# Kernel optimization log

Hardware: AMD Instinct MI355X
Metric: run time of the kernel (lower is better)

Reference implementation:

```python
import jax, jax.numpy as jnp
import numpy as np

B = 4; S_L = 512; WIN = 256; SCH = 3; CCH = 128; F = 8; P = 4; RNN = 128; FC = 256
L1 = (WIN - F + 1) // P          # after conv1 + pool1
L2 = (L1 - F + 1) // P           # after conv2 + pool2
D1 = L2 * CCH                    # flattened conv feature dim fed to GRU


def _conv1d(x, w, b):
    # x: (N, W, Cin), w: (F, Cin, Cout), VALID, stride 1 (matches keras Conv1D)
    return jax.lax.conv_general_dilated(x, w, (1,), 'VALID', dimension_numbers=('NWC', 'WIO', 'NWC')) + b


def _maxpool(x, p):
    return jax.lax.reduce_window(x, -jnp.inf, jax.lax.max, (1, p, 1), (1, p, 1), 'VALID')


def _gru(x, h0, mask, W, U, b):
    # keras GRU v2 (reset_after=True). b[0]=input bias, b[1]=recurrent bias.
    # Masked steps carry state through (keras semantics: output==state for GRU).
    u = U.shape[0]
    xg = x @ W + b[0]  # (B, T, 3u) precomputed input projections
    br = b[1]

    def step(h, inp):
        xt, mt = inp  # (B, 3u), (B,)
        rg = h @ U + br
        z = jax.nn.sigmoid(xt[:, :u] + rg[:, :u])
        r = jax.nn.sigmoid(xt[:, u:2 * u] + rg[:, u:2 * u])
        hh = jnp.tanh(xt[:, 2 * u:] + r * rg[:, 2 * u:])
        hn = z * h + (1.0 - z) * hh
        hn = jnp.where(mt[:, None], hn, h)
        return hn, hn

    _, ys = jax.lax.scan(step, h0, (jnp.swapaxes(xg, 0, 1), jnp.swapaxes(mask, 0, 1)))
    return jnp.swapaxes(ys, 0, 1)  # (B, T, u)


def _bidir(x, m, hf, hb, Wf, Uf, bf, Wb, Ub, bb):
    # Bidirectional(merge='concat'); backward layer sees reversed inputs+mask,
    # its output is reversed back to align with time (keras behaviour).
    yf = _gru(x, hf, m, Wf, Uf, bf)
    yb = _gru(x[:, ::-1], hb, m[:, ::-1], Wb, Ub, bb)[:, ::-1]
    return jnp.concatenate([yf, yb], axis=-1)


def _forward(x, state1_f, state1_b, state2_f, state2_b,
             conv1_w, conv1_b, conv2_w, conv2_b,
             g1f_W, g1f_U, g1f_b, g1b_W, g1b_U, g1b_b,
             g2f_W, g2f_U, g2f_b, g2b_W, g2b_U, g2b_b,
             d1_w, d1_b, d2_w, d2_b, d3_w, d3_b, m):
    bsz = x.shape[0]
    h = x.reshape(bsz * S_L, WIN, SCH)
    h = _maxpool(jax.nn.leaky_relu(_conv1d(h, conv1_w, conv1_b), 0.2), P)
    h = _maxpool(jax.nn.leaky_relu(_conv1d(h, conv2_w, conv2_b), 0.2), P)
    h = h.reshape(bsz, S_L, D1)
    h = _bidir(h, m, state1_f, state1_b, g1f_W, g1f_U, g1f_b, g1b_W, g1b_U, g1b_b)
    h = _bidir(h, m, state2_f, state2_b, g2f_W, g2f_U, g2f_b, g2b_W, g2b_U, g2b_b)
    # keras layers.Attention(use_scale=False): dot-product self attention,
    # key mask -> -1e9 on scores, query mask -> zero outputs.
    scores = jnp.einsum('btd,bsd->bts', h, h)
    scores = jnp.where(m[:, None, :], scores, -1e9)
    h = jnp.einsum('bts,bsd->btd', jax.nn.softmax(scores, axis=-1), h)
    h = h * m[:, :, None].astype(h.dtype)
    h = jax.nn.leaky_relu(h @ d1_w + d1_b, 0.2)   # dropout is identity at inference
    h = jax.nn.leaky_relu(h @ d2_w + d2_b, 0.2)
    return (h @ d3_w + d3_b)[..., 0]              # squeeze -> (B, s_l)


def setup_inputs() -> dict:
    key = jax.random.key(0)
    ks = jax.random.split(key, 32)
    g = lambda k, s: jax.random.normal(k, s, jnp.float32) * 0.05
    inp = {}
    inp['x'] = jax.random.normal(ks[0], (B, S_L, WIN, SCH), jnp.float32)
    inp['m'] = jax.random.randint(ks[1], (B, S_L), 0, 2) > 0
    inp['state1_f'] = jax.random.uniform(ks[2], (B, RNN), jnp.float32, -1.0, 1.0)
    inp['state1_b'] = jax.random.uniform(ks[3], (B, RNN), jnp.float32, -1.0, 1.0)
    inp['state2_f'] = jax.random.uniform(ks[4], (B, RNN), jnp.float32, -1.0, 1.0)
    inp['state2_b'] = jax.random.uniform(ks[5], (B, RNN), jnp.float32, -1.0, 1.0)
    inp['conv1_w'] = g(ks[6], (F, SCH, CCH)); inp['conv1_b'] = jnp.zeros((CCH,), jnp.float32)
    inp['conv2_w'] = g(ks[7], (F, CCH, CCH)); inp['conv2_b'] = jnp.zeros((CCH,), jnp.float32)
    i = 8
    for nm, din in (('g1f', D1), ('g1b', D1), ('g2f', 2 * RNN), ('g2b', 2 * RNN)):
        inp[nm + '_W'] = g(ks[i], (din, 3 * RNN))
        inp[nm + '_U'] = g(ks[i + 1], (RNN, 3 * RNN))
        inp[nm + '_b'] = jnp.zeros((2, 3 * RNN), jnp.float32)
        i += 2
    inp['d1_w'] = g(ks[i], (2 * RNN, FC)); inp['d1_b'] = jnp.zeros((FC,), jnp.float32)
    inp['d2_w'] = g(ks[i + 1], (FC, FC)); inp['d2_b'] = jnp.zeros((FC,), jnp.float32)
    inp['d3_w'] = g(ks[i + 2], (FC, 1)); inp['d3_b'] = jnp.zeros((1,), jnp.float32)
    return inp


def reference(x, m, state1_f, state1_b, state2_f, state2_b,
              conv1_w, conv1_b, conv2_w, conv2_b,
              g1f_W, g1f_U, g1f_b, g1b_W, g1b_U, g1b_b,
              g2f_W, g2f_U, g2f_b, g2b_W, g2b_U, g2b_b,
              d1_w, d1_b, d2_w, d2_b, d3_w, d3_b):
    return _forward(x, state1_f, state1_b, state2_f, state2_b,
                    conv1_w, conv1_b, conv2_w, conv2_b,
                    g1f_W, g1f_U, g1f_b, g1b_W, g1b_U, g1b_b,
                    g2f_W, g2f_U, g2f_b, g2b_W, g2b_U, g2b_b,
                    d1_w, d1_b, d2_w, d2_b, d3_w, d3_b, m)
```

## Files before the change

kernel.cpp:

```cpp
#include <hip/hip_runtime.h>

#define LRELU(v) ((v) > 0.f ? (v) : 0.2f * (v))

typedef float f32x4 __attribute__((ext_vector_type(4)));
typedef __bf16 bf16x8 __attribute__((ext_vector_type(8)));
typedef unsigned short ushort8v __attribute__((ext_vector_type(8)));
typedef unsigned int u32x2 __attribute__((ext_vector_type(2)));

__device__ __forceinline__ unsigned short f2bf(float f) {
    unsigned int u = __float_as_uint(f);
    u += 0x7fffu + ((u >> 16) & 1u);
    return (unsigned short)(u >> 16);
}
__device__ __forceinline__ float bf2f(unsigned short h) {
    return __uint_as_float(((unsigned int)h) << 16);
}
__device__ __forceinline__ float sigmoid_fast(float x) {
    float e = __builtin_amdgcn_exp2f(-x * 1.442695041f);
    return __builtin_amdgcn_rcpf(1.f + e);
}
__device__ __forceinline__ float tanh_fast(float x) {
    float e = __builtin_amdgcn_exp2f(x * 2.885390082f);
    return 1.f - 2.f * __builtin_amdgcn_rcpf(e + 1.f);
}
__device__ __forceinline__ float dpp_add_xor1(float v) {
    int r = __builtin_amdgcn_mov_dpp(__float_as_int(v), 0xB1, 0xF, 0xF, true);
    return v + __int_as_float(r);
}
__device__ __forceinline__ float dpp_add_xor2(float v) {
    int r = __builtin_amdgcn_mov_dpp(__float_as_int(v), 0x4E, 0xF, 0xF, true);
    return v + __int_as_float(r);
}

__device__ __forceinline__ void wtpack(const float* __restrict__ W,
                                       unsigned short* __restrict__ h,
                                       unsigned short* __restrict__ l, int K,
                                       int N, long idx) {
    int n = (int)(idx / K), k = (int)(idx % K);
    float v = W[(long)k * N + n];
    unsigned short hi = f2bf(v);
    h[idx] = hi;
    l[idx] = f2bf(v - bf2f(hi));
}
__device__ __forceinline__ void ugpack(const float* __restrict__ U,
                                       float* __restrict__ up, int widx) {
    int quad = widx >> 11;
    int rem = widx & 2047;
    int t = rem >> 2, i = rem & 3;
    int g = quad >> 3, q = quad & 7;
    int c = t >> 2, kq = t & 3;
    up[widx] = U[(long)(kq * 32 + q * 4 + i) * 384 + g * 128 + c];
}

__global__ __launch_bounds__(256) void prepack_all(
    const float* __restrict__ w2, unsigned short* __restrict__ bth,
    unsigned short* __restrict__ btl, const float* __restrict__ g1fW,
    unsigned short* __restrict__ wt1fh, unsigned short* __restrict__ wt1fl,
    const float* __restrict__ g1bW, unsigned short* __restrict__ wt1bh,
    unsigned short* __restrict__ wt1bl, const float* __restrict__ g2fW,
    unsigned short* __restrict__ wt2fh, unsigned short* __restrict__ wt2fl,
    const float* __restrict__ g2bW, unsigned short* __restrict__ wt2bh,
    unsigned short* __restrict__ wt2bl, const float* __restrict__ g1fU,
    float* __restrict__ up1f, const float* __restrict__ g1bU,
    float* __restrict__ up1b, const float* __restrict__ g2fU,
    float* __restrict__ up2f, const float* __restrict__ g2bU,
    float* __restrict__ up2b, const float* __restrict__ d1w,
    unsigned short* __restrict__ d1th, unsigned short* __restrict__ d1tl,
    const float* __restrict__ d2w, unsigned short* __restrict__ d2th,
    unsigned short* __restrict__ d2tl, const unsigned int* __restrict__ mraw,
    int* __restrict__ mi) {
    const int bid = blockIdx.x, tid = threadIdx.x;
    if (bid < 512) {
        int idx = bid * 256 + tid;
        int c = idx >> 10, k = idx & 1023;
        float v = w2[k * 128 + c];
        unsigned short hi = f2bf(v);
        bth[(long)c * 1024 + k] = hi;
        btl[(long)c * 1024 + k] = f2bf(v - bf2f(hi));
    } else if (bid < 3008) {
        wtpack(g1fW, wt1fh, wt1fl, 1664, 384, (long)(bid - 512) * 256 + tid);
    } else if (bid < 5504) {
        wtpack(g1bW, wt1bh, wt1bl, 1664, 384, (long)(bid - 3008) * 256 + tid);
    } else if (bid < 5888) {
        wtpack(g2fW, wt2fh, wt2fl, 256, 384, (long)(bid - 5504) * 256 + tid);
    } else if (bid < 6272) {
        wtpack(g2bW, wt2bh, wt2bl, 256, 384, (long)(bid - 5888) * 256 + tid);
    } else if (bid < 6464) {
        ugpack(g1fU, up1f, (bid - 6272) * 256 + tid);
    } else if (bid < 6656) {
        ugpack(g1bU, up1b, (bid - 6464) * 256 + tid);
    } else if (bid < 6848) {
        ugpack(g2fU, up2f, (bid - 6656) * 256 + tid);
    } else if (bid < 7040) {
        ugpack(g2bU, up2b, (bid - 6848) * 256 + tid);
    } else if (bid < 7296) {
        wtpack(d1w, d1th, d1tl, 256, 256, (long)(bid - 7040) * 256 + tid);
    } else if (bid < 7552) {
        wtpack(d2w, d2th, d2tl, 256, 256, (long)(bid - 7296) * 256 + tid);
    } else {
        __shared__ int flag;
        if (tid == 0) flag = 0;
        __syncthreads();
        unsigned a = mraw[tid * 2], bb = mraw[tid * 2 + 1];
        if (a > 1u || bb > 1u) flag = 1;
        __syncthreads();
        if (flag) {
            const unsigned char* b8 = (const unsigned char*)mraw;
            for (int i = tid; i < 2048; i += 256) mi[i] = b8[i] ? 1 : 0;
        } else {
            for (int i = tid; i < 2048; i += 256) mi[i] = mraw[i] ? 1 : 0;
        }
    }
}

__global__ __launch_bounds__(256) void conv_kernel(
    const float* __restrict__ x, const float* __restrict__ w1,
    const float* __restrict__ b1, const unsigned short* __restrict__ bth,
    const unsigned short* __restrict__ btl, const float* __restrict__ b2,
    unsigned short* __restrict__ feat_h, unsigned short* __restrict__ feat_l) {
    __shared__ float xs[3][256];
    __shared__ __align__(16) unsigned short p1h[72 * 128];
    __shared__ __align__(16) unsigned short p1l[72 * 128];
    long s = blockIdx.x;
    int tid = threadIdx.x;
    const float* xp = x + s * 768;
    for (int i = tid; i < 768; i += 256) xs[i % 3][i / 3] = xp[i];
    for (int i = tid; i < 10 * 128; i += 256) {
        p1h[62 * 128 + i] = 0;
        p1l[62 * 128 + i] = 0;
    }
    __syncthreads();

    {
        int ch = tid & 127;
        int half = tid >> 7;
        float w1r[24];
#pragma unroll
        for (int fc = 0; fc < 24; fc++) w1r[fc] = w1[fc * 128 + ch];
        float bias1 = b1[ch];
        for (int po = half; po < 62; po += 2) {
            int p0 = po * 4;
            float a0 = bias1, a1 = bias1, a2 = bias1, a3 = bias1;
#pragma unroll
            for (int c = 0; c < 3; c++) {
                float xv[11];
#pragma unroll
                for (int q = 0; q < 11; q++) xv[q] = xs[c][p0 + q];
#pragma unroll
                for (int f = 0; f < 8; f++) {
                    float w = w1r[f * 3 + c];
                    a0 = fmaf(xv[f + 0], w, a0);
                    a1 = fmaf(xv[f + 1], w, a1);
                    a2 = fmaf(xv[f + 2], w, a2);
                    a3 = fmaf(xv[f + 3], w, a3);
                }
            }
            float m01 = fmaxf(LRELU(a0), LRELU(a1));
            float m23 = fmaxf(LRELU(a2), LRELU(a3));
            float v = fmaxf(m01, m23);
            unsigned short hi = f2bf(v);
            unsigned short lo = f2bf(v - bf2f(hi));
            int cs = ch ^ ((po & 7) << 3);
            p1h[po * 128 + cs] = hi;
            p1l[po * 128 + cs] = lo;
        }
    }
    __syncthreads();

    const int l = tid & 63, w = tid >> 6;
    const int r = l & 15, g = l >> 4;
    f32x4 acc[4][2];
    const f32x4 zz = {0.f, 0.f, 0.f, 0.f};
#pragma unroll
    for (int m = 0; m < 4; m++) {
        acc[m][0] = zz;
        acc[m][1] = zz;
    }
#pragma unroll 2
    for (int ks = 0; ks < 32; ks++) {
        const int f = ks >> 2;
        const int cin0 = ((ks & 3) << 5) + (g << 3);
        bf16x8 bh[2], bl[2];
#pragma unroll
        for (int n = 0; n < 2; n++) {
            const int c = ((w << 1) + n) * 16 + r;
            const long bo = (long)c * 1024 + (ks << 5) + (g << 3);
            bh[n] = __builtin_bit_cast(bf16x8, *(const ushort8v*)(bth + bo));
            bl[n] = __builtin_bit_cast(bf16x8, *(const ushort8v*)(btl + bo));
        }
        bf16x8 ah[4], al[4];
#pragma unroll
        for (int m = 0; m < 4; m++) {
            const int row = m * 16 + r + f;
            const int col = cin0 ^ ((row & 7) << 3);
            const int off = row * 128 + col;
            ah[m] = __builtin_bit_cast(bf16x8, *(const ushort8v*)(p1h + off));
            al[m] = __builtin_bit_cast(bf16x8, *(const ushort8v*)(p1l + off));
        }
#pragma unroll
        for (int m = 0; m < 4; m++) {
#pragma unroll
            for (int n = 0; n < 2; n++) {
                acc[m][n] = __builtin_amdgcn_mfma_f32_16x16x32_bf16(ah[m], bh[n], acc[m][n], 0, 0, 0);
                acc[m][n] = __builtin_amdgcn_mfma_f32_16x16x32_bf16(ah[m], bl[n], acc[m][n], 0, 0, 0);
                acc[m][n] = __builtin_amdgcn_mfma_f32_16x16x32_bf16(al[m], bh[n], acc[m][n], 0, 0, 0);
            }
        }
    }
#pragma unroll
    for (int m = 0; m < 4; m++) {
        const int j = m * 4 + g;
        if (j < 13) {
#pragma unroll
            for (int n = 0; n < 2; n++) {
                const int ch = ((w << 1) + n) * 16 + r;
                const float bias = b2[ch];
                float v0 = LRELU(acc[m][n].x + bias);
                float v1 = LRELU(acc[m][n].y + bias);
                float v2 = LRELU(acc[m][n].z + bias);
                float v3 = LRELU(acc[m][n].w + bias);
                float v = fmaxf(fmaxf(v0, v1), fmaxf(v2, v3));
                unsigned short hi = f2bf(v);
                feat_h[s * 1664 + j * 128 + ch] = hi;
                feat_l[s * 1664 + j * 128 + ch] = f2bf(v - bf2f(hi));
            }
        }
    }
}

__global__ __launch_bounds__(256) void gemm_proj(
    const unsigned short* __restrict__ Agh, const unsigned short* __restrict__ Agl,
    const unsigned short* __restrict__ B0h, const unsigned short* __restrict__ B0l,
    const unsigned short* __restrict__ B1h, const unsigned short* __restrict__ B1l,
    const float* __restrict__ bias0, const float* __restrict__ bias1,
    float* __restrict__ C0, float* __restrict__ C1, int M, int N, int K) {
    const int z = blockIdx.z;
    const unsigned short* __restrict__ Bth = z ? B1h : B0h;
    const unsigned short* __restrict__ Btl = z ? B1l : B0l;
    const float* __restrict__ bias = z ? bias1 : bias0;
    float* __restrict__ C = z ? C1 : C0;
    __shared__ __align__(16) unsigned short Ahs[2][64 * 32];
    __shared__ __align__(16) unsigned short Als[2][64 * 32];
    const int tid = threadIdx.x;
    const int w = tid >> 6, l = tid & 63, r = l & 15, g = l >> 4;
    const int m0 = blockIdx.y * 64, n0 = blockIdx.x * 64;
    const int col = n0 + w * 16 + r;
    const int srow = tid >> 2, sgq = tid & 3;
    f32x4 acc[4];
    const f32x4 zzv = {0.f, 0.f, 0.f, 0.f};
#pragma unroll
    for (int m = 0; m < 4; m++) acc[m] = zzv;

    const long abase = (long)(m0 + srow) * K + ((sgq ^ (srow & 3)) << 3);
    auto stage = [&](int k0, int buf) {
        __builtin_amdgcn_global_load_lds(
            (const __attribute__((address_space(1))) void*)(Agh + abase + k0),
            (__attribute__((address_space(3))) void*)&Ahs[buf][tid * 8], 16, 0, 0);
        __builtin_amdgcn_global_load_lds(
            (const __attribute__((address_space(1))) void*)(Agl + abase + k0),
            (__attribute__((address_space(3))) void*)&Als[buf][tid * 8], 16, 0, 0);
    };
    stage(0, 0);
    const long bbase = (long)col * K + g * 8;
    ushort8v bhc = *(const ushort8v*)(Bth + bbase);
    ushort8v blc = *(const ushort8v*)(Btl + bbase);

    for (int k0 = 0; k0 < K; k0 += 32) {
        const int buf = (k0 >> 5) & 1;
        asm volatile("s_waitcnt vmcnt(0)" ::: "memory");
        __builtin_amdgcn_s_barrier();
        ushort8v nbh, nbl;
        if (k0 + 32 < K) {
            stage(k0 + 32, buf ^ 1);
            nbh = *(const ushort8v*)(Bth + bbase + k0 + 32);
            nbl = *(const ushort8v*)(Btl + bbase + k0 + 32);
        }
        bf16x8 bh = __builtin_bit_cast(bf16x8, bhc);
        bf16x8 bl = __builtin_bit_cast(bf16x8, blc);
#pragma unroll
        for (int m = 0; m < 4; m++) {
            const int arow = m * 16 + r;
            const int aoff = arow * 32 + ((g ^ (arow & 3)) << 3);
            bf16x8 ah = __builtin_bit_cast(bf16x8, *(const ushort8v*)(&Ahs[buf][aoff]));
            bf16x8 al = __builtin_bit_cast(bf16x8, *(const ushort8v*)(&Als[buf][aoff]));
            acc[m] = __builtin_amdgcn_mfma_f32_16x16x32_bf16(ah, bh, acc[m], 0, 0, 0);
            acc[m] = __builtin_amdgcn_mfma_f32_16x16x32_bf16(ah, bl, acc[m], 0, 0, 0);
            acc[m] = __builtin_amdgcn_mfma_f32_16x16x32_bf16(al, bh, acc[m], 0, 0, 0);
        }
        bhc = nbh;
        blc = nbl;
    }
    const float bv = bias[col];
#pragma unroll
    for (int m = 0; m < 4; m++) {
#pragma unroll
        for (int q = 0; q < 4; q++) {
            const int row = m0 + m * 16 + g * 4 + q;
            C[(long)row * N + col] = acc[m][q] + bv;
        }
    }
}

__global__ __launch_bounds__(256) void gemm_scores(
    const unsigned short* __restrict__ Hh, const unsigned short* __restrict__ Hl,
    const int* __restrict__ mask, float* __restrict__ S) {
    const int bz = blockIdx.z;
    const unsigned short* __restrict__ Agh = Hh + (long)bz * 512 * 256;
    const unsigned short* __restrict__ Agl = Hl + (long)bz * 512 * 256;
    float* __restrict__ C = S + (long)bz * 512 * 512;
    const int K = 256, N = 512;
    __shared__ __align__(16) unsigned short Ahs[2][64 * 32];
    __shared__ __align__(16) unsigned short Als[2][64 * 32];
    const int tid = threadIdx.x;
    const int w = tid >> 6, l = tid & 63, r = l & 15, g = l >> 4;
    const int m0 = blockIdx.y * 64, n0 = blockIdx.x * 64;
    const int col = n0 + w * 16 + r;
    const int srow = tid >> 2, sgq = tid & 3;
    f32x4 acc[4];
    const f32x4 zzv = {0.f, 0.f, 0.f, 0.f};
#pragma unroll
    for (int m = 0; m < 4; m++) acc[m] = zzv;

    const long abase = (long)(m0 + srow) * K + ((sgq ^ (srow & 3)) << 3);
    auto stage = [&](int k0, int buf) {
        __builtin_amdgcn_global_load_lds(
            (const __attribute__((address_space(1))) void*)(Agh + abase + k0),
            (__attribute__((address_space(3))) void*)&Ahs[buf][tid * 8], 16, 0, 0);
        __builtin_amdgcn_global_load_lds(
            (const __attribute__((address_space(1))) void*)(Agl + abase + k0),
            (__attribute__((address_space(3))) void*)&Als[buf][tid * 8], 16, 0, 0);
    };
    stage(0, 0);
    const long bbase = (long)col * K + g * 8;
    ushort8v bhc = *(const ushort8v*)(Agh + bbase);
    ushort8v blc = *(const ushort8v*)(Agl + bbase);

    for (int k0 = 0; k0 < K; k0 += 32) {
        const int buf = (k0 >> 5) & 1;
        asm volatile("s_waitcnt vmcnt(0)" ::: "memory");
        __builtin_amdgcn_s_barrier();
        ushort8v nbh, nbl;
        if (k0 + 32 < K) {
            stage(k0 + 32, buf ^ 1);
            nbh = *(const ushort8v*)(Agh + bbase + k0 + 32);
            nbl = *(const ushort8v*)(Agl + bbase + k0 + 32);
        }
        bf16x8 bh = __builtin_bit_cast(bf16x8, bhc);
        bf16x8 bl = __builtin_bit_cast(bf16x8, blc);
#pragma unroll
        for (int m = 0; m < 4; m++) {
            const int arow = m * 16 + r;
            const int aoff = arow * 32 + ((g ^ (arow & 3)) << 3);
            bf16x8 ah = __builtin_bit_cast(bf16x8, *(const ushort8v*)(&Ahs[buf][aoff]));
            bf16x8 al = __builtin_bit_cast(bf16x8, *(const ushort8v*)(&Als[buf][aoff]));
            acc[m] = __builtin_amdgcn_mfma_f32_16x16x32_bf16(ah, bh, acc[m], 0, 0, 0);
            acc[m] = __builtin_amdgcn_mfma_f32_16x16x32_bf16(ah, bl, acc[m], 0, 0, 0);
            acc[m] = __builtin_amdgcn_mfma_f32_16x16x32_bf16(al, bh, acc[m], 0, 0, 0);
        }
        bhc = nbh;
        blc = nbl;
    }
    const int mk = mask[bz * 512 + col];
#pragma unroll
    for (int m = 0; m < 4; m++) {
#pragma unroll
        for (int q = 0; q < 4; q++) {
            const int row = m0 + m * 16 + g * 4 + q;
            float v = acc[m][q];
            C[(long)row * N + col] = mk ? v : -1e9f;
        }
    }
}

template <int ACT, int QMASK>
__global__ __launch_bounds__(256) void gemm_v3(
    const unsigned short* __restrict__ Agh, const unsigned short* __restrict__ Agl,
    const unsigned short* __restrict__ Bth, const unsigned short* __restrict__ Btl,
    const float* __restrict__ bias, const int* __restrict__ qmask,
    unsigned short* __restrict__ Ch, unsigned short* __restrict__ Cl,
    long sA, long sB, long sC, int M, int N, int K) {
    const int bz = blockIdx.z;
    Agh += (long)bz * sA;
    Agl += (long)bz * sA;
    Bth += (long)bz * sB;
    Btl += (long)bz * sB;
    Ch += (long)bz * sC;
    Cl += (long)bz * sC;
    __shared__ __align__(16) unsigned short Ahs[2][64 * 32];
    __shared__ __align__(16) unsigned short Als[2][64 * 32];
    const int tid = threadIdx.x;
    const int w = tid >> 6, l = tid & 63, r = l & 15, g = l >> 4;
    const int m0 = blockIdx.y * 64, n0 = blockIdx.x * 64;
    const int col = n0 + w * 16 + r;
    const int srow = tid >> 2, sgq = tid & 3;
    f32x4 acc[4];
    const f32x4 zzv = {0.f, 0.f, 0.f, 0.f};
#pragma unroll
    for (int m = 0; m < 4; m++) acc[m] = zzv;

    const long abase = (long)(m0 + srow) * K + ((sgq ^ (srow & 3)) << 3);
    auto stage = [&](int k0, int buf) {
        __builtin_amdgcn_global_load_lds(
            (const __attribute__((address_space(1))) void*)(Agh + abase + k0),
            (__attribute__((address_space(3))) void*)&Ahs[buf][tid * 8], 16, 0, 0);
        __builtin_amdgcn_global_load_lds(
            (const __attribute__((address_space(1))) void*)(Agl + abase + k0),
            (__attribute__((address_space(3))) void*)&Als[buf][tid * 8], 16, 0, 0);
    };
    stage(0, 0);
    const long bbase = (long)col * K + g * 8;
    ushort8v bhc = *(const ushort8v*)(Bth + bbase);
    ushort8v blc = *(const ushort8v*)(Btl + bbase);

    for (int k0 = 0; k0 < K; k0 += 32) {
        const int buf = (k0 >> 5) & 1;
        asm volatile("s_waitcnt vmcnt(0)" ::: "memory");
        __builtin_amdgcn_s_barrier();
        ushort8v nbh, nbl;
        if (k0 + 32 < K) {
            stage(k0 + 32, buf ^ 1);
            nbh = *(const ushort8v*)(Bth + bbase + k0 + 32);
            nbl = *(const ushort8v*)(Btl + bbase + k0 + 32);
        }
        bf16x8 bh = __builtin_bit_cast(bf16x8, bhc);
        bf16x8 bl = __builtin_bit_cast(bf16x8, blc);
#pragma unroll
        for (int m = 0; m < 4; m++) {
            const int arow = m * 16 + r;
            const int aoff = arow * 32 + ((g ^ (arow & 3)) << 3);
            bf16x8 ah = __builtin_bit_cast(bf16x8, *(const ushort8v*)(&Ahs[buf][aoff]));
            bf16x8 al = __builtin_bit_cast(bf16x8, *(const ushort8v*)(&Als[buf][aoff]));
            acc[m] = __builtin_amdgcn_mfma_f32_16x16x32_bf16(ah, bh, acc[m], 0, 0, 0);
            acc[m] = __builtin_amdgcn_mfma_f32_16x16x32_bf16(ah, bl, acc[m], 0, 0, 0);
            acc[m] = __builtin_amdgcn_mfma_f32_16x16x32_bf16(al, bh, acc[m], 0, 0, 0);
        }
        bhc = nbh;
        blc = nbl;
    }
    const float bv = bias ? bias[col] : 0.f;
#pragma unroll
    for (int m = 0; m < 4; m++) {
#pragma unroll
        for (int q = 0; q < 4; q++) {
            const int row = m0 + m * 16 + g * 4 + q;
            float v = acc[m][q] + bv;
            if (ACT == 1) v = LRELU(v);
            if (QMASK) v *= (float)qmask[bz * M + row];
            unsigned short hi = f2bf(v);
            Ch[(long)row * N + col] = hi;
            Cl[(long)row * N + col] = f2bf(v - bf2f(hi));
        }
    }
}

__global__ __launch_bounds__(256) void transpose_hl(
    const unsigned short* __restrict__ inh, const unsigned short* __restrict__ inl,
    unsigned short* __restrict__ outh, unsigned short* __restrict__ outl) {
    __shared__ unsigned short th[32][33], tl[32][33];
    const int b = blockIdx.z;
    const int s0 = blockIdx.x * 32, d0 = blockIdx.y * 32;
    const unsigned short* ih = inh + (long)b * 512 * 256;
    const unsigned short* il = inl + (long)b * 512 * 256;
    unsigned short* oh = outh + (long)b * 256 * 512;
    unsigned short* ol = outl + (long)b * 256 * 512;
    const int tx = threadIdx.x & 31, ty = threadIdx.x >> 5;
#pragma unroll
    for (int i = 0; i < 4; i++) {
        int s = s0 + ty + i * 8;
        th[ty + i * 8][tx] = ih[(long)s * 256 + d0 + tx];
        tl[ty + i * 8][tx] = il[(long)s * 256 + d0 + tx];
    }
    __syncthreads();
#pragma unroll
    for (int i = 0; i < 4; i++) {
        int d = d0 + ty + i * 8;
        oh[(long)d * 512 + s0 + tx] = th[tx][ty + i * 8];
        ol[(long)d * 512 + s0 + tx] = tl[tx][ty + i * 8];
    }
}

__global__ __launch_bounds__(256) void softmax_kernel(
    const float* __restrict__ S, unsigned short* __restrict__ Ph,
    unsigned short* __restrict__ Pl) {
    long row = blockIdx.x;
    const float* p = S + row * 512;
    int tid = threadIdx.x;
    __shared__ float red[8];
    float v0 = p[tid], v1 = p[tid + 256];
    float mx = fmaxf(v0, v1);
#pragma unroll
    for (int off = 32; off; off >>= 1) mx = fmaxf(mx, __shfl_down(mx, off));
    if ((tid & 63) == 0) red[tid >> 6] = mx;
    __syncthreads();
    mx = fmaxf(fmaxf(red[0], red[1]), fmaxf(red[2], red[3]));
    float e0 = expf(v0 - mx), e1 = expf(v1 - mx);
    float sm = e0 + e1;
#pragma unroll
    for (int off = 32; off; off >>= 1) sm += __shfl_down(sm, off);
    if ((tid & 63) == 0) red[4 + (tid >> 6)] = sm;
    __syncthreads();
    float inv = 1.f / (red[4] + red[5] + red[6] + red[7]);
    float w0 = e0 * inv, w1 = e1 * inv;
    unsigned short h0 = f2bf(w0), h1 = f2bf(w1);
    Ph[row * 512 + tid] = h0;
    Pl[row * 512 + tid] = f2bf(w0 - bf2f(h0));
    Ph[row * 512 + tid + 256] = h1;
    Pl[row * 512 + tid + 256] = f2bf(w1 - bf2f(h1));
}

#define D4(a0, a1, hv, uv)           \
    a0 = fmaf(hv.x, uv.x, a0);       \
    a1 = fmaf(hv.y, uv.y, a1);       \
    a0 = fmaf(hv.z, uv.z, a0);       \
    a1 = fmaf(hv.w, uv.w, a1);

__global__ __launch_bounds__(512, 2) void gru_kernel(
    const float* __restrict__ xgf, const float* __restrict__ xgb,
    const float* __restrict__ Upf, const float* __restrict__ Upb,
    const float* __restrict__ brf, const float* __restrict__ brb,
    const float* __restrict__ h0f, const float* __restrict__ h0b,
    const int* __restrict__ mask, unsigned short* __restrict__ outh,
    unsigned short* __restrict__ outl) {
    int b = blockIdx.x & 3;
    int dir = blockIdx.x >> 2;
    const float* __restrict__ xg = dir ? xgb : xgf;
    const float* __restrict__ Up = dir ? Upb : Upf;
    const float* __restrict__ br = dir ? brb : brf;
    const float* __restrict__ h0 = dir ? h0b : h0f;
    const int tid = threadIdx.x;
    const int c = tid >> 2;
    const int kq = tid & 3;

    __shared__ __align__(16) float xs[2][16 * 384];
    __shared__ __align__(16) float hsh[2][144];
    __shared__ __align__(16) unsigned int histp[16][128];
    __shared__ unsigned long long mwords[8];

    auto stage = [&](int cc, int bufi) {
#pragma unroll
        for (int i = 0; i < 3; i++) {
            int g = i * 512 + tid;
            int j = g / 96;
            int col = (g - j * 96) * 4;
            int ts = cc * 16 + j;
            int t = dir ? (511 - ts) : ts;
            const float* src = xg + ((long)(b * 512 + t)) * 384 + col;
            __builtin_amdgcn_global_load_lds(
                (const __attribute__((address_space(1))) void*)src,
                (__attribute__((address_space(3))) void*)&xs[bufi][g * 4], 16, 0, 0);
        }
    };
    stage(0, 0);

    const float* ub = Up + (tid << 2);
    f32x4 uz0 = *(const f32x4*)(ub + 0 * 2048);
    f32x4 uz1 = *(const f32x4*)(ub + 1 * 2048);
    f32x4 uz2 = *(const f32x4*)(ub + 2 * 2048);
    f32x4 uz3 = *(const f32x4*)(ub + 3 * 2048);
    f32x4 uz4 = *(const f32x4*)(ub + 4 * 2048);
    f32x4 uz5 = *(const f32x4*)(ub + 5 * 2048);
    f32x4 uz6 = *(const f32x4*)(ub + 6 * 2048);
    f32x4 uz7 = *(const f32x4*)(ub + 7 * 2048);
    f32x4 ur0 = *(const f32x4*)(ub + 8 * 2048);
    f32x4 ur1 = *(const f32x4*)(ub + 9 * 2048);
    f32x4 ur2 = *(const f32x4*)(ub + 10 * 2048);
    f32x4 ur3 = *(const f32x4*)(ub + 11 * 2048);
    f32x4 ur4 = *(const f32x4*)(ub + 12 * 2048);
    f32x4 ur5 = *(const f32x4*)(ub + 13 * 2048);
    f32x4 ur6 = *(const f32x4*)(ub + 14 * 2048);
    f32x4 ur7 = *(const f32x4*)(ub + 15 * 2048);
    f32x4 uh0 = *(const f32x4*)(ub + 16 * 2048);
    f32x4 uh1 = *(const f32x4*)(ub + 17 * 2048);
    f32x4 uh2 = *(const f32x4*)(ub + 18 * 2048);
    f32x4 uh3 = *(const f32x4*)(ub + 19 * 2048);
    f32x4 uh4 = *(const f32x4*)(ub + 20 * 2048);
    f32x4 uh5 = *(const f32x4*)(ub + 21 * 2048);
    f32x4 uh6 = *(const f32x4*)(ub + 22 * 2048);
    f32x4 uh7 = *(const f32x4*)(ub + 23 * 2048);

    float br3[3];
#pragma unroll
    for (int g = 0; g < 3; g++) br3[g] = br[g * 128 + c];

    float hreg = h0[b * 128 + c];
    if (kq == 0) hsh[0][c + (c >> 5) * 4] = hreg;
    if (tid < 64) {
#pragma unroll
        for (int w = 0; w < 8; w++) {
            int idx = w * 64 + tid;
            int t = dir ? (511 - idx) : idx;
            unsigned long long bm = __ballot(mask[b * 512 + t] != 0);
            if (tid == 0) mwords[w] = bm;
        }
    }
    asm volatile("s_waitcnt lgkmcnt(0)" ::: "memory");
    __builtin_amdgcn_s_barrier();

    int cur = 0;
    for (int cc = 0; cc < 32; cc++) {
        asm volatile("s_waitcnt vmcnt(0)" ::: "memory");
        if (cc < 31) stage(cc + 1, (cc + 1) & 1);
        __builtin_amdgcn_s_barrier();
        const float* xb = xs[cc & 1];
        unsigned mwbits = (unsigned)((mwords[cc >> 2] >> ((cc & 3) * 16)) & 0xffffull);
#pragma unroll 1
        for (int jj = 0; jj < 16; jj++) {
            if ((mwbits >> jj) & 1) {
                const float* hp = &hsh[cur][kq * 36];
                float4 h0v = *(const float4*)(hp + 0);
                float4 h1v = *(const float4*)(hp + 4);
                float4 h2v = *(const float4*)(hp + 8);
                float4 h3v = *(const float4*)(hp + 12);
                float4 h4v = *(const float4*)(hp + 16);
                float4 h5v = *(const float4*)(hp + 20);
                float4 h6v = *(const float4*)(hp + 24);
                float4 h7v = *(const float4*)(hp + 28);
                float az0 = 0.f, az1 = 0.f, ar0 = 0.f, ar1 = 0.f, ah0 = 0.f, ah1 = 0.f;
                D4(az0, az1, h0v, uz0) D4(az0, az1, h1v, uz1)
                D4(az0, az1, h2v, uz2) D4(az0, az1, h3v, uz3)
                D4(az0, az1, h4v, uz4) D4(az0, az1, h5v, uz5)
                D4(az0, az1, h6v, uz6) D4(az0, az1, h7v, uz7)
                D4(ar0, ar1, h0v, ur0) D4(ar0, ar1, h1v, ur1)
                D4(ar0, ar1, h2v, ur2) D4(ar0, ar1, h3v, ur3)
                D4(ar0, ar1, h4v, ur4) D4(ar0, ar1, h5v, ur5)
                D4(ar0, ar1, h6v, ur6) D4(ar0, ar1, h7v, ur7)
                D4(ah0, ah1, h0v, uh0) D4(ah0, ah1, h1v, uh1)
                D4(ah0, ah1, h2v, uh2) D4(ah0, ah1, h3v, uh3)
                D4(ah0, ah1, h4v, uh4) D4(ah0, ah1, h5v, uh5)
                D4(ah0, ah1, h6v, uh6) D4(ah0, ah1, h7v, uh7)
                float rgz = dpp_add_xor2(dpp_add_xor1(az0 + az1));
                float rgr = dpp_add_xor2(dpp_add_xor1(ar0 + ar1));
                float rgh = dpp_add_xor2(dpp_add_xor1(ah0 + ah1));
                if (kq == 0) {
                    float xz = xb[jj * 384 + c];
                    float xr = xb[jj * 384 + 128 + c];
                    float xh = xb[jj * 384 + 256 + c];
                    float z = sigmoid_fast(xz + rgz + br3[0]);
                    float r_ = sigmoid_fast(xr + rgr + br3[1]);
                    float hc = tanh_fast(fmaf(r_, rgh + br3[2], xh));
                    float hn = fmaf(z, hreg - hc, hc);
                    hreg = hn;
                    hsh[cur ^ 1][c + (c >> 5) * 4] = hn;
                    unsigned short hh = f2bf(hn);
                    histp[jj][c] = (unsigned)hh |
                                   ((unsigned)f2bf(hn - bf2f(hh)) << 16);
                }
                asm volatile("s_waitcnt lgkmcnt(0)" ::: "memory");
                __builtin_amdgcn_s_barrier();
                cur ^= 1;
            } else {
                if (kq == 0) {
                    unsigned short hh = f2bf(hreg);
                    histp[jj][c] = (unsigned)hh |
                                   ((unsigned)f2bf(hreg - bf2f(hh)) << 16);
                }
            }
        }
        asm volatile("s_waitcnt lgkmcnt(0)" ::: "memory");
        __builtin_amdgcn_s_barrier();
        {
            int fj = tid >> 5, fc = (tid & 31) << 2;
            int ts2 = cc * 16 + fj;
            int tf = dir ? (511 - ts2) : ts2;
            long ob = ((long)(b * 512 + tf)) * 256 + dir * 128 + fc;
            uint4 hp4 = *(const uint4*)&histp[fj][fc];
            u32x2 ph, pl;
            ph.x = (hp4.x & 0xffffu) | (hp4.y << 16);
            ph.y = (hp4.z & 0xffffu) | (hp4.w << 16);
            pl.x = (hp4.x >> 16) | (hp4.y & 0xffff0000u);
            pl.y = (hp4.z >> 16) | (hp4.w & 0xffff0000u);
            *(u32x2*)(outh + ob) = ph;
            *(u32x2*)(outl + ob) = pl;
        }
    }
}

__global__ __launch_bounds__(256) void final_kernel(
    const unsigned short* __restrict__ fh, const unsigned short* __restrict__ fl,
    const float* __restrict__ w, const float* __restrict__ b,
    float* __restrict__ out) {
    int row = blockIdx.x * 4 + (threadIdx.x >> 6);
    int lane = threadIdx.x & 63;
    const unsigned short* ah = fh + (long)row * 256;
    const unsigned short* al = fl + (long)row * 256;
    float acc = 0.f;
#pragma unroll
    for (int i = 0; i < 4; i++) {
        int idx = lane + i * 64;
        float a = bf2f(ah[idx]) + bf2f(al[idx]);
        acc = fmaf(a, w[idx], acc);
    }
#pragma unroll
    for (int off = 32; off; off >>= 1) acc += __shfl_down(acc, off);
    if (lane == 0) out[row] = acc + b[0];
}

extern "C" void kernel_launch(void* const* d_in, const int* in_sizes, int n_in,
                              void* d_out, int out_size, void* d_ws,
                              size_t ws_size, hipStream_t stream) {
    const float* x = (const float*)d_in[0];
    const unsigned int* mraw = (const unsigned int*)d_in[1];
    const float* s1f = (const float*)d_in[2];
    const float* s1b = (const float*)d_in[3];
    const float* s2f = (const float*)d_in[4];
    const float* s2b = (const float*)d_in[5];
    const float* c1w = (const float*)d_in[6];
    const float* c1b = (const float*)d_in[7];
    const float* c2w = (const float*)d_in[8];
    const float* c2b = (const float*)d_in[9];
    const float* g1fW = (const float*)d_in[10];
    const float* g1fU = (const float*)d_in[11];
    const float* g1fb = (const float*)d_in[12];
    const float* g1bW = (const float*)d_in[13];
    const float* g1bU = (const float*)d_in[14];
    const float* g1bb = (const float*)d_in[15];
    const float* g2fW = (const float*)d_in[16];
    const float* g2fU = (const float*)d_in[17];
    const float* g2fb = (const float*)d_in[18];
    const float* g2bW = (const float*)d_in[19];
    const float* g2bU = (const float*)d_in[20];
    const float* g2bb = (const float*)d_in[21];
    const float* d1w = (const float*)d_in[22];
    const float* d1b = (const float*)d_in[23];
    const float* d2w = (const float*)d_in[24];
    const float* d2b = (const float*)d_in[25];
    const float* d3w = (const float*)d_in[26];
    const float* d3b = (const float*)d_in[27];
    float* out = (float*)d_out;

    float* ws = (float*)d_ws;
    size_t off = 0;
    auto take = [&](size_t n) {
        float* p = ws + off;
        off += (n + 63) & ~(size_t)63;
        return p;
    };
    int* mask_i = (int*)take(2048);
    unsigned short* feat_h = (unsigned short*)take(2048UL * 1664 / 2);
    unsigned short* feat_l = (unsigned short*)take(2048UL * 1664 / 2);
    float* xg1f = take(2048UL * 384);
    float* xg1b = take(2048UL * 384);
    unsigned short* gru1h = (unsigned short*)take(2048UL * 128);
    unsigned short* gru1l = (unsigned short*)take(2048UL * 128);
    float* xg2f = take(2048UL * 384);
    float* xg2b = take(2048UL * 384);
    unsigned short* gru2h = (unsigned short*)take(2048UL * 128);
    unsigned short* gru2l = (unsigned short*)take(2048UL * 128);
    unsigned short* ght = (unsigned short*)take(2048UL * 128);
    unsigned short* glt = (unsigned short*)take(2048UL * 128);
    float* sc = take(4UL * 512 * 512);
    unsigned short* scH = (unsigned short*)take(4UL * 512 * 256);
    unsigned short* scL = (unsigned short*)take(4UL * 512 * 256);
    unsigned short* attnH = (unsigned short*)take(2048UL * 128);
    unsigned short* attnL = (unsigned short*)take(2048UL * 128);
    unsigned short* fc1H = (unsigned short*)take(2048UL * 128);
    unsigned short* fc1L = (unsigned short*)take(2048UL * 128);
    unsigned short* fc2H = (unsigned short*)take(2048UL * 128);
    unsigned short* fc2L = (unsigned short*)take(2048UL * 128);
    unsigned short* bth = (unsigned short*)take(65536);
    unsigned short* btl = (unsigned short*)take(65536);
    unsigned short* wt1fh = (unsigned short*)take(319488);
    unsigned short* wt1fl = (unsigned short*)take(319488);
    unsigned short* wt1bh = (unsigned short*)take(319488);
    unsigned short* wt1bl = (unsigned short*)take(319488);
    unsigned short* wt2fh = (unsigned short*)take(49152);
    unsigned short* wt2fl = (unsigned short*)take(49152);
    unsigned short* wt2bh = (unsigned short*)take(49152);
    unsigned short* wt2bl = (unsigned short*)take(49152);
    unsigned short* d1th = (unsigned short*)take(32768);
    unsigned short* d1tl = (unsigned short*)take(32768);
    unsigned short* d2th = (unsigned short*)take(32768);
    unsigned short* d2tl = (unsigned short*)take(32768);
    float* up1f = take(49152);
    float* up1b = take(49152);
    float* up2f = take(49152);
    float* up2b = take(49152);

    prepack_all<<<7553, 256, 0, stream>>>(
        c2w, bth, btl, g1fW, wt1fh, wt1fl, g1bW, wt1bh, wt1bl, g2fW, wt2fh,
        wt2fl, g2bW, wt2bh, wt2bl, g1fU, up1f, g1bU, up1b, g2fU, up2f, g2bU,
        up2b, d1w, d1th, d1tl, d2w, d2th, d2tl, mraw, mask_i);
    conv_kernel<<<2048, 256, 0, stream>>>(x, c1w, c1b, bth, btl, c2b, feat_h, feat_l);

    gemm_proj<<<dim3(6, 32, 2), 256, 0, stream>>>(
        feat_h, feat_l, wt1fh, wt1fl, wt1bh, wt1bl, g1fb, g1bb, xg1f, xg1b,
        2048, 384, 1664);
    gru_kernel<<<8, 512, 0, stream>>>(xg1f, xg1b, up1f, up1b, g1fb + 384,
                                      g1bb + 384, s1f, s1b, mask_i, gru1h, gru1l);

    gemm_proj<<<dim3(6, 32, 2), 256, 0, stream>>>(
        gru1h, gru1l, wt2fh, wt2fl, wt2bh, wt2bl, g2fb, g2bb, xg2f, xg2b,
        2048, 384, 256);
    gru_kernel<<<8, 512, 0, stream>>>(xg2f, xg2b, up2f, up2b, g2fb + 384,
                                      g2bb + 384, s2f, s2b, mask_i, gru2h, gru2l);

    transpose_hl<<<dim3(16, 8, 4), 256, 0, stream>>>(gru2h, gru2l, ght, glt);
    gemm_scores<<<dim3(8, 8, 4), 256, 0, stream>>>(gru2h, gru2l, mask_i, sc);
    softmax_kernel<<<2048, 256, 0, stream>>>(sc, scH, scL);
    gemm_v3<0, 1><<<dim3(4, 8, 4), 256, 0, stream>>>(
        scH, scL, ght, glt, nullptr, mask_i, attnH, attnL,
        512L * 512, 256L * 512, 512L * 256, 512, 256, 512);
    gemm_v3<1, 0><<<dim3(4, 32, 1), 256, 0, stream>>>(
        attnH, attnL, d1th, d1tl, d1b, nullptr, fc1H, fc1L,
        0, 0, 0, 2048, 256, 256);
    gemm_v3<1, 0><<<dim3(4, 32, 1), 256, 0, stream>>>(
        fc1H, fc1L, d2th, d2tl, d2b, nullptr, fc2H, fc2L,
        0, 0, 0, 2048, 256, 256);
    final_kernel<<<512, 256, 0, stream>>>(fc2H, fc2L, d3w, d3b, out);
}
```

Baseline: 630.5 us.

## Fuse softmax into attention context GEMM and fuse dense2 with final projection

Replaces the separate softmax kernel and the batched P@V GEMM with a single kernel that computes row max and sum per wave, then recomputes exp on the fly while feeding MFMA, so the bf16 hi/lo probability matrices are never materialised. It also fuses the second dense layer with the final 256->1 projection, keeping fc1 tiles in LDS and reducing to the output directly. This removes two launches and several intermediate global round trips. In exchange the new kernels launch far fewer blocks (32), and the context kernel reads V operands directly from global memory without LDS staging, which risks lower parallelism and bandwidth use.

Result: slower. 715.1 us (+13.4%).

```diff
diff --git a/kernel.cpp b/kernel.cpp
--- a/kernel.cpp
+++ b/kernel.cpp
@@ -22,6 +22,9 @@
 __device__ __forceinline__ float tanh_fast(float x) {
     float e = __builtin_amdgcn_exp2f(x * 2.885390082f);
     return 1.f - 2.f * __builtin_amdgcn_rcpf(e + 1.f);
+}
+__device__ __forceinline__ float exp_fast(float x) {
+    return __builtin_amdgcn_exp2f(x * 1.442695041f);
 }
 __device__ __forceinline__ float dpp_add_xor1(float v) {
     int r = __builtin_amdgcn_mov_dpp(__float_as_int(v), 0xB1, 0xF, 0xF, true);
@@ -372,20 +375,12 @@
     }
 }
 
-template <int ACT, int QMASK>
+template <int ACT>
 __global__ __launch_bounds__(256) void gemm_v3(
     const unsigned short* __restrict__ Agh, const unsigned short* __restrict__ Agl,
     const unsigned short* __restrict__ Bth, const unsigned short* __restrict__ Btl,
-    const float* __restrict__ bias, const int* __restrict__ qmask,
-    unsigned short* __restrict__ Ch, unsigned short* __restrict__ Cl,
-    long sA, long sB, long sC, int M, int N, int K) {
-    const int bz = blockIdx.z;
-    Agh += (long)bz * sA;
-    Agl += (long)bz * sA;
-    Bth += (long)bz * sB;
-    Btl += (long)bz * sB;
-    Ch += (long)bz * sC;
-    Cl += (long)bz * sC;
+    const float* __restrict__ bias, unsigned short* __restrict__ Ch,
+    unsigned short* __restrict__ Cl, int M, int N, int K) {
     __shared__ __align__(16) unsigned short Ahs[2][64 * 32];
     __shared__ __align__(16) unsigned short Als[2][64 * 32];
     const int tid = threadIdx.x;
@@ -445,7 +440,6 @@
             const int row = m0 + m * 16 + g * 4 + q;
             float v = acc[m][q] + bv;
             if (ACT == 1) v = LRELU(v);
-            if (QMASK) v *= (float)qmask[bz * M + row];
             unsigned short hi = f2bf(v);
             Ch[(long)row * N + col] = hi;
             Cl[(long)row * N + col] = f2bf(v - bf2f(hi));
@@ -479,33 +473,186 @@
     }
 }
 
-__global__ __launch_bounds__(256) void softmax_kernel(
-    const float* __restrict__ S, unsigned short* __restrict__ Ph,
-    unsigned short* __restrict__ Pl) {
-    long row = blockIdx.x;
-    const float* p = S + row * 512;
-    int tid = threadIdx.x;
-    __shared__ float red[8];
-    float v0 = p[tid], v1 = p[tid + 256];
-    float mx = fmaxf(v0, v1);
-#pragma unroll
-    for (int off = 32; off; off >>= 1) mx = fmaxf(mx, __shfl_down(mx, off));
-    if ((tid & 63) == 0) red[tid >> 6] = mx;
+__global__ __launch_bounds__(256) void ctx_flash(
+    const float* __restrict__ S, const unsigned short* __restrict__ ght,
+    const unsigned short* __restrict__ glt, const int* __restrict__ mask,
+    unsigned short* __restrict__ attnH, unsigned short* __restrict__ attnL) {
+    const int b = blockIdx.z, qt = blockIdx.x;
+    const int tid = threadIdx.x;
+    const int w = tid >> 6, l = tid & 63, r = l & 15, g = l >> 4;
+    const int qbase = qt * 64 + w * 16;
+    const float* Sw = S + (long)b * 512 * 512 + (long)qbase * 512;
+
+    float mkeep = 0.f, ikeep = 0.f;
+#pragma unroll 1
+    for (int q = 0; q < 16; q++) {
+        const float* row = Sw + (long)q * 512 + l * 8;
+        float4 v0 = *(const float4*)row;
+        float4 v1 = *(const float4*)(row + 4);
+        float mx = fmaxf(fmaxf(fmaxf(v0.x, v0.y), fmaxf(v0.z, v0.w)),
+                         fmaxf(fmaxf(v1.x, v1.y), fmaxf(v1.z, v1.w)));
+#pragma unroll
+        for (int off = 32; off; off >>= 1) mx = fmaxf(mx, __shfl_xor(mx, off));
+        float se = exp_fast(v0.x - mx) + exp_fast(v0.y - mx) +
+                   exp_fast(v0.z - mx) + exp_fast(v0.w - mx) +
+                   exp_fast(v1.x - mx) + exp_fast(v1.y - mx) +
+                   exp_fast(v1.z - mx) + exp_fast(v1.w - mx);
+#pragma unroll
+        for (int off = 32; off; off >>= 1) se += __shfl_xor(se, off);
+        if (q == r) {
+            mkeep = mx;
+            ikeep = __builtin_amdgcn_rcpf(se);
+        }
+    }
+
+    f32x4 o[16];
+    const f32x4 zzv = {0.f, 0.f, 0.f, 0.f};
+#pragma unroll
+    for (int dt = 0; dt < 16; dt++) o[dt] = zzv;
+    const float* Sp = S + (long)b * 512 * 512 + (long)(qbase + r) * 512;
+    const unsigned short* gb = ght + (long)b * 131072;
+    const unsigned short* lb = glt + (long)b * 131072;
+#pragma unroll 1
+    for (int kt = 0; kt < 8; kt++) {
+        const int k0 = kt * 64;
+        const float* pp = Sp + k0 + 8 * g;
+        float4 a0 = *(const float4*)pp;
+        float4 a1 = *(const float4*)(pp + 4);
+        float4 a2 = *(const float4*)(pp + 32);
+        float4 a3 = *(const float4*)(pp + 36);
+        float pv[16] = {a0.x, a0.y, a0.z, a0.w, a1.x, a1.y, a1.z, a1.w,
+                        a2.x, a2.y, a2.z, a2.w, a3.x, a3.y, a3.z, a3.w};
+        ushort8v ph0, pl0, ph1, pl1;
+#pragma unroll
+        for (int j = 0; j < 8; j++) {
+            float p = exp_fast(pv[j] - mkeep) * ikeep;
+            unsigned short hi = f2bf(p);
+            ph0[j] = hi;
+            pl0[j] = f2bf(p - bf2f(hi));
+            float p2 = exp_fast(pv[8 + j] - mkeep) * ikeep;
+            unsigned short hi2 = f2bf(p2);
+            ph1[j] = hi2;
+            pl1[j] = f2bf(p2 - bf2f(hi2));
+        }
+        bf16x8 pah0 = __builtin_bit_cast(bf16x8, ph0);
+        bf16x8 pal0 = __builtin_bit_cast(bf16x8, pl0);
+        bf16x8 pah1 = __builtin_bit_cast(bf16x8, ph1);
+        bf16x8 pal1 = __builtin_bit_cast(bf16x8, pl1);
+#pragma unroll
+        for (int ks2 = 0; ks2 < 2; ks2++) {
+            bf16x8 pah = ks2 ? pah1 : pah0;
+            bf16x8 pal = ks2 ? pal1 : pal0;
+#pragma unroll
+            for (int dt = 0; dt < 16; dt++) {
+                const long bo = (long)(dt * 16 + r) * 512 + k0 + ks2 * 32 + 8 * g;
+                bf16x8 bh = __builtin_bit_cast(bf16x8, *(const ushort8v*)(gb + bo));
+                bf16x8 bl = __builtin_bit_cast(bf16x8, *(const ushort8v*)(lb + bo));
+                o[dt] = __builtin_amdgcn_mfma_f32_16x16x32_bf16(pah, bh, o[dt], 0, 0, 0);
+                o[dt] = __builtin_amdgcn_mfma_f32_16x16x32_bf16(pah, bl, o[dt], 0, 0, 0);
+                o[dt] = __builtin_amdgcn_mfma_f32_16x16x32_bf16(pal, bh, o[dt], 0, 0, 0);
+            }
+        }
+    }
+#pragma unroll
+    for (int reg = 0; reg < 4; reg++) {
+        const int qglob = qbase + 4 * g + reg;
+        const float qm = (float)mask[b * 512 + qglob];
+        unsigned short* oh = attnH + ((long)(b * 512 + qglob)) * 256;
+        unsigned short* ol = attnL + ((long)(b * 512 + qglob)) * 256;
+#pragma unroll
+        for (int dt = 0; dt < 16; dt++) {
+            float v = o[dt][reg] * qm;
+            unsigned short hi = f2bf(v);
+            oh[dt * 16 + r] = hi;
+            ol[dt * 16 + r] = f2bf(v - bf2f(hi));
+        }
+    }
+}
+
+__global__ __launch_bounds__(256) void head2_kernel(
+    const unsigned short* __restrict__ fc1H, const unsigned short* __restrict__ fc1L,
+    const unsigned short* __restrict__ d2th, const unsigned short* __restrict__ d2tl,
+    const float* __restrict__ d2b, const float* __restrict__ d3w,
+    const float* __restrict__ d3b, float* __restrict__ out) {
+    __shared__ __align__(16) unsigned short Ah[64 * 256];
+    __shared__ __align__(16) unsigned short Al[64 * 256];
+    __shared__ float fpart[4][64];
+    const int tid = threadIdx.x;
+    const int w = tid >> 6, l = tid & 63, r = l & 15, g = l >> 4;
+    const int m0 = blockIdx.x * 64;
+#pragma unroll
+    for (int it = 0; it < 8; it++) {
+        int gi = it * 256 + tid;
+        int row = gi >> 5, slot = gi & 31;
+        int scol = (slot ^ (row & 7)) * 8;
+        const long so = (long)(m0 + row) * 256 + scol;
+        __builtin_amdgcn_global_load_lds(
+            (const __attribute__((address_space(1))) void*)(fc1H + so),
+            (__attribute__((address_space(3))) void*)&Ah[gi * 8], 16, 0, 0);
+        __builtin_amdgcn_global_load_lds(
+            (const __attribute__((address_space(1))) void*)(fc1L + so),
+            (__attribute__((address_space(3))) void*)&Al[gi * 8], 16, 0, 0);
+    }
+    asm volatile("s_waitcnt vmcnt(0)" ::: "memory");
     __syncthreads();
-    mx = fmaxf(fmaxf(red[0], red[1]), fmaxf(red[2], red[3]));
-    float e0 = expf(v0 - mx), e1 = expf(v1 - mx);
-    float sm = e0 + e1;
-#pragma unroll
-    for (int off = 32; off; off >>= 1) sm += __shfl_down(sm, off);
-    if ((tid & 63) == 0) red[4 + (tid >> 6)] = sm;
+
+    float fs[4][4];
+#pragma unroll
+    for (int m = 0; m < 4; m++)
+#pragma unroll
+        for (int q = 0; q < 4; q++) fs[m][q] = 0.f;
+
+#pragma unroll 1
+    for (int s = 0; s < 4; s++) {
+        const int col = s * 64 + w * 16 + r;
+        const long bbase = (long)col * 256 + g * 8;
+        f32x4 acc[4];
+        const f32x4 zzv = {0.f, 0.f, 0.f, 0.f};
+#pragma unroll
+        for (int m = 0; m < 4; m++) acc[m] = zzv;
+#pragma unroll
+        for (int ks = 0; ks < 8; ks++) {
+            bf16x8 bh = __builtin_bit_cast(bf16x8, *(const ushort8v*)(d2th + bbase + ks * 32));
+            bf16x8 bl = __builtin_bit_cast(bf16x8, *(const ushort8v*)(d2tl + bbase + ks * 32));
+#pragma unroll
+            for (int m = 0; m < 4; m++) {
+                const int arow = m * 16 + r;
+                const int aoff = arow * 256 + (((ks * 4 + g) ^ (arow & 7)) << 3);
+                bf16x8 ah = __builtin_bit_cast(bf16x8, *(const ushort8v*)(Ah + aoff));
+                bf16x8 al = __builtin_bit_cast(bf16x8, *(const ushort8v*)(Al + aoff));
+                acc[m] = __builtin_amdgcn_mfma_f32_16x16x32_bf16(ah, bh, acc[m], 0, 0, 0);
+                acc[m] = __builtin_amdgcn_mfma_f32_16x16x32_bf16(ah, bl, acc[m], 0, 0, 0);
+                acc[m] = __builtin_amdgcn_mfma_f32_16x16x32_bf16(al, bh, acc[m], 0, 0, 0);
+            }
+        }
+        const float bv = d2b[col];
+        const float w3 = d3w[col];
+#pragma unroll
+        for (int m = 0; m < 4; m++)
+#pragma unroll
+            for (int q = 0; q < 4; q++) {
+                float v = LRELU(acc[m][q] + bv);
+                fs[m][q] = fmaf(v, w3, fs[m][q]);
+            }
+    }
+#pragma unroll
+    for (int off = 1; off < 16; off <<= 1)
+#pragma unroll
+        for (int m = 0; m < 4; m++)
+#pragma unroll
+            for (int q = 0; q < 4; q++) fs[m][q] += __shfl_xor(fs[m][q], off);
+    if (r == 0) {
+#pragma unroll
+        for (int m = 0; m < 4; m++)
+#pragma unroll
+            for (int q = 0; q < 4; q++) fpart[w][m * 16 + 4 * g + q] = fs[m][q];
+    }
     __syncthreads();
-    float inv = 1.f / (red[4] + red[5] + red[6] + red[7]);
-    float w0 = e0 * inv, w1 = e1 * inv;
-    unsigned short h0 = f2bf(w0), h1 = f2bf(w1);
-    Ph[row * 512 + tid] = h0;
-    Pl[row * 512 + tid] = f2bf(w0 - bf2f(h0));
-    Ph[row * 512 + tid + 256] = h1;
-    Pl[row * 512 + tid + 256] = f2bf(w1 - bf2f(h1));
+    if (tid < 64) {
+        float tot = fpart[0][tid] + fpart[1][tid] + fpart[2][tid] +
+                    fpart[3][tid] + d3b[0];
+        out[m0 + tid] = tot;
+    }
 }
 
 #define D4(a0, a1, hv, uv)           \
@@ -675,26 +822,6 @@
     }
 }
 
-__global__ __launch_bounds__(256) void final_kernel(
-    const unsigned short* __restrict__ fh, const unsigned short* __restrict__ fl,
-    const float* __restrict__ w, const float* __restrict__ b,
-    float* __restrict__ out) {
-    int row = blockIdx.x * 4 + (threadIdx.x >> 6);
-    int lane = threadIdx.x & 63;
-    const unsigned short* ah = fh + (long)row * 256;
-    const unsigned short* al = fl + (long)row * 256;
-    float acc = 0.f;
-#pragma unroll
-    for (int i = 0; i < 4; i++) {
-        int idx = lane + i * 64;
-        float a = bf2f(ah[idx]) + bf2f(al[idx]);
-        acc = fmaf(a, w[idx], acc);
-    }
-#pragma unroll
-    for (int off = 32; off; off >>= 1) acc += __shfl_down(acc, off);
-    if (lane == 0) out[row] = acc + b[0];
-}
-
 extern "C" void kernel_launch(void* const* d_in, const int* in_sizes, int n_in,
                               void* d_out, int out_size, void* d_ws,
                               size_t ws_size, hipStream_t stream) {
@@ -749,14 +876,10 @@
     unsigned short* ght = (unsigned short*)take(2048UL * 128);
     unsigned short* glt = (unsigned short*)take(2048UL * 128);
     float* sc = take(4UL * 512 * 512);
-    unsigned short* scH = (unsigned short*)take(4UL * 512 * 256);
-    unsigned short* scL = (unsigned short*)take(4UL * 512 * 256);
     unsigned short* attnH = (unsigned short*)take(2048UL * 128);
     unsigned short* attnL = (unsigned short*)take(2048UL * 128);
     unsigned short* fc1H = (unsigned short*)take(2048UL * 128);
     unsigned short* fc1L = (unsigned short*)take(2048UL * 128);
-    unsigned short* fc2H = (unsigned short*)take(2048UL * 128);
-    unsigned short* fc2L = (unsigned short*)take(2048UL * 128);
     unsigned short* bth = (unsigned short*)take(65536);
     unsigned short* btl = (unsigned short*)take(65536);
     unsigned short* wt1fh = (unsigned short*)take(319488);
@@ -796,15 +919,9 @@
 
     transpose_hl<<<dim3(16, 8, 4), 256, 0, stream>>>(gru2h, gru2l, ght, glt);
     gemm_scores<<<dim3(8, 8, 4), 256, 0, stream>>>(gru2h, gru2l, mask_i, sc);
-    softmax_kernel<<<2048, 256, 0, stream>>>(sc, scH, scL);
-    gemm_v3<0, 1><<<dim3(4, 8, 4), 256, 0, stream>>>(
-        scH, scL, ght, glt, nullptr, mask_i, attnH, attnL,
-        512L * 512, 256L * 512, 512L * 256, 512, 256, 512);
-    gemm_v3<1, 0><<<dim3(4, 32, 1), 256, 0, stream>>>(
-        attnH, attnL, d1th, d1tl, d1b, nullptr, fc1H, fc1L,
-        0, 0, 0, 2048, 256, 256);
-    gemm_v3<1, 0><<<dim3(4, 32, 1), 256, 0, stream>>>(
-        fc1H, fc1L, d2th, d2tl, d2b, nullptr, fc2H, fc2L,
-        0, 0, 0, 2048, 256, 256);
-    final_kernel<<<512, 256, 0, stream>>>(fc2H, fc2L, d3w, d3b, out);
-}
+    ctx_flash<<<dim3(8, 1, 4), 256, 0, stream>>>(sc, ght, glt, mask_i, attnH, attnL);
+    gemm_v3<1><<<dim3(4, 32, 1), 256, 0, stream>>>(
+        attnH, attnL, d1th, d1tl, d1b, fc1H, fc1L, 2048, 256, 256);
+    head2_kernel<<<32, 256, 0, stream>>>(fc1H, fc1L, d2th, d2tl, d2b, d3w,
+                                         d3b, out);
+}
```
